# Kernel optimization log

Hardware: AMD Instinct MI355X
Metric: run time of the kernel (lower is better)

The kernel has to match this reference:

```python
import jax, jax.numpy as jnp
import numpy as np

N_NODES = 100000


def gcn_conv(x, W, b, src, dst, n_nodes):
    """PyG GCNConv: add self-loops, symmetric deg^-1/2 normalization,
    linear transform then gather->scale->scatter-add, plus bias."""
    h = x @ W  # [N, out] - transform first (small GEMM), propagate after
    loop = jnp.arange(n_nodes, dtype=src.dtype)
    s = jnp.concatenate([src, loop])  # sources incl. self-loops
    d = jnp.concatenate([dst, loop])  # targets incl. self-loops
    deg = jax.ops.segment_sum(jnp.ones_like(d, dtype=h.dtype), d,
                              num_segments=n_nodes)  # in-degree on augmented graph
    dinv = jnp.where(deg > 0, jax.lax.rsqrt(deg), 0.0)
    norm = dinv[s] * dinv[d]  # [E+N]
    msg = h[s] * norm[:, None]  # gather + per-edge scale
    out = jax.ops.segment_sum(msg, d, num_segments=n_nodes)  # scatter-add
    return out + b


def setup_inputs() -> dict:
    key = jax.random.key(0)
    ks = jax.random.split(key, 8)
    in_dim, hid = 128, 128
    n_edges = 1600000
    x = jax.random.normal(ks[0], (N_NODES, in_dim), dtype=jnp.float32)
    edge_index = jax.random.randint(ks[1], (2, n_edges), 0, N_NODES, dtype=jnp.int64)
    s1 = 1.0 / np.sqrt(in_dim)
    s2 = 1.0 / np.sqrt(hid)
    W1 = jax.random.uniform(ks[2], (in_dim, hid), jnp.float32, -s1, s1)
    b1 = jnp.zeros((hid,), jnp.float32)
    W2 = jax.random.uniform(ks[3], (hid, 2), jnp.float32, -s2, s2)
    b2 = jnp.zeros((2,), jnp.float32)
    W_skip = jax.random.uniform(ks[4], (in_dim, 2), jnp.float32, -s1, s1)
    b_skip = jnp.zeros((2,), jnp.float32)
    return {"x": x, "edge_index": edge_index, "W1": W1, "b1": b1,
            "W2": W2, "b2": b2, "W_skip": W_skip, "b_skip": b_skip}


def reference(x, edge_index, W1, b1, W2, b2, W_skip, b_skip):
    src, dst = edge_index[0], edge_index[1]
    h = gcn_conv(x, W1, b1, src, dst, N_NODES)
    h = jax.nn.relu(h)
    # dropout is identity in eval mode (training=False)
    out = gcn_conv(h, W2, b2, src, dst, N_NODES)
    out = out + x @ W_skip + b_skip
    return out
```

## Files before the change

kernel.cpp:

```cpp
#include <hip/hip_runtime.h>

#define NN 100000
#define NB 196
#define BSHIFT 9
#define BMASK 511

typedef __attribute__((ext_vector_type(8))) short short8;
typedef __attribute__((ext_vector_type(4))) float f32x4;
typedef __attribute__((ext_vector_type(2))) float f32x2;

__device__ __forceinline__ unsigned short f2bf(float f) {
  union { float f; unsigned int u; } v;
  v.f = f;
  unsigned int r = (v.u + 0x7fffu + ((v.u >> 16) & 1u)) >> 16;
  return (unsigned short)r;
}
__device__ __forceinline__ float bf_lo(unsigned int u) {
  union { unsigned int u; float f; } v;
  v.u = u << 16;
  return v.f;
}
__device__ __forceinline__ float bf_hi(unsigned int u) {
  union { unsigned int u; float f; } v;
  v.u = u & 0xffff0000u;
  return v.f;
}
__device__ __forceinline__ f32x2 bfpair(unsigned int u) {
  union { unsigned int u; float f; } lo, hi;
  lo.u = u << 16;
  hi.u = u & 0xffff0000u;
  f32x2 r;
  r.x = lo.f;
  r.y = hi.f;
  return r;
}

union SMem {
  struct {
    int cnt_l[NB];
    int start_l[NB];
    int gbase[NB];
    int wsum2[8];
    unsigned int stage[4096];
    int addr[4096];
  } b;
  struct {
    unsigned short Bs[16384];
    float Ws[256];
  } g;
};

__global__ __launch_bounds__(512) void k_phase1(const int* __restrict__ src,
                                                const int* __restrict__ dst, int E,
                                                int cap, int* __restrict__ bcur,
                                                unsigned int* __restrict__ bkt,
                                                const float* __restrict__ x,
                                                const float* __restrict__ W1,
                                                const float* __restrict__ W_skip,
                                                unsigned short* __restrict__ hA16,
                                                float* __restrict__ skipout, int N,
                                                int nbatch) {
  __shared__ __align__(16) SMem sm;
  const int t = threadIdx.x;
  const int lane = t & 63, wid = t >> 6;

  if ((int)blockIdx.x < nbatch) {
    for (int i = t; i < NB; i += 512) sm.b.cnt_l[i] = 0;
    __syncthreads();
    const int bi = blockIdx.x;
    const int e0 = bi << 12;
    unsigned int ent[8];
    int bb[8], pp[8];
#pragma unroll
    for (int j = 0; j < 8; ++j) {
      int e = e0 + j * 512 + t;
      if (e < E) {
        int d = dst[e], s = src[e];
        bb[j] = d >> BSHIFT;
        ent[j] = ((unsigned int)s << BSHIFT) | (unsigned int)(d & BMASK);
        pp[j] = atomicAdd(&sm.b.cnt_l[bb[j]], 1);
      } else {
        bb[j] = -1;
      }
    }
    __syncthreads();
    int v = (t < NB) ? sm.b.cnt_l[t] : 0;
    if (t < NB) sm.b.gbase[t] = atomicAdd(&bcur[t], v);
    int incl = v;
#pragma unroll
    for (int off = 1; off < 64; off <<= 1) {
      int u = __shfl_up(incl, off);
      if (lane >= off) incl += u;
    }
    if (lane == 63) sm.b.wsum2[wid] = incl;
    __syncthreads();
    int wpre = 0;
#pragma unroll
    for (int j = 0; j < 8; ++j) wpre += (j < wid) ? sm.b.wsum2[j] : 0;
    int tot = sm.b.wsum2[0] + sm.b.wsum2[1] + sm.b.wsum2[2] + sm.b.wsum2[3] +
              sm.b.wsum2[4] + sm.b.wsum2[5] + sm.b.wsum2[6] + sm.b.wsum2[7];
    if (t < NB) sm.b.start_l[t] = wpre + incl - v;
    __syncthreads();
#pragma unroll
    for (int j = 0; j < 8; ++j) {
      if (bb[j] >= 0) {
        int slot = sm.b.start_l[bb[j]] + pp[j];
        sm.b.stage[slot] = ent[j];
        sm.b.addr[slot] = bb[j] * cap + sm.b.gbase[bb[j]] + pp[j];
      }
    }
    __syncthreads();
    for (int s2 = t; s2 < tot; s2 += 512) bkt[sm.b.addr[s2]] = sm.b.stage[s2];
    return;
  }

  const int rb = blockIdx.x - nbatch;
#pragma unroll
  for (int it = 0; it < 4; ++it) {
    int idx = t + it * 512;
    int l2 = idx & 63, f = idx >> 6;
    int nt = f >> 2, ks = f & 3;
    int nn = nt * 16 + (l2 & 15);
    int k0 = ks * 32 + (l2 >> 4) * 8;
    unsigned short tmp[8];
#pragma unroll
    for (int j = 0; j < 8; ++j) tmp[j] = f2bf(W1[(k0 + j) * 128 + nn]);
    *(uint4*)&sm.g.Bs[idx * 8] = *(uint4*)tmp;
  }
  if (t < 256) sm.g.Ws[t] = W_skip[t];
  __syncthreads();

  const int m = lane & 15, q = lane >> 4;
  const int grow = rb * 128 + wid * 16 + m;
  const bool valid = grow < N;
  const float* xp = &x[(size_t)(valid ? grow : 0) * 128];

  f32x4 acc[8];
#pragma unroll
  for (int nt = 0; nt < 8; ++nt) acc[nt] = (f32x4){0.f, 0.f, 0.f, 0.f};
  float sk0 = 0.f, sk1 = 0.f;

#pragma unroll
  for (int ks = 0; ks < 4; ++ks) {
    short8 a;
    const int kb = ks * 32 + q * 8;
    if (valid) {
      const float* p = xp + kb;
      float4 f0 = *(const float4*)p;
      float4 f1 = *(const float4*)(p + 4);
      a[0] = (short)f2bf(f0.x); a[1] = (short)f2bf(f0.y);
      a[2] = (short)f2bf(f0.z); a[3] = (short)f2bf(f0.w);
      a[4] = (short)f2bf(f1.x); a[5] = (short)f2bf(f1.y);
      a[6] = (short)f2bf(f1.z); a[7] = (short)f2bf(f1.w);
      sk0 += f0.x * sm.g.Ws[(kb + 0) * 2] + f0.y * sm.g.Ws[(kb + 1) * 2] +
             f0.z * sm.g.Ws[(kb + 2) * 2] + f0.w * sm.g.Ws[(kb + 3) * 2] +
             f1.x * sm.g.Ws[(kb + 4) * 2] + f1.y * sm.g.Ws[(kb + 5) * 2] +
             f1.z * sm.g.Ws[(kb + 6) * 2] + f1.w * sm.g.Ws[(kb + 7) * 2];
      sk1 += f0.x * sm.g.Ws[(kb + 0) * 2 + 1] + f0.y * sm.g.Ws[(kb + 1) * 2 + 1] +
             f0.z * sm.g.Ws[(kb + 2) * 2 + 1] + f0.w * sm.g.Ws[(kb + 3) * 2 + 1] +
             f1.x * sm.g.Ws[(kb + 4) * 2 + 1] + f1.y * sm.g.Ws[(kb + 5) * 2 + 1] +
             f1.z * sm.g.Ws[(kb + 6) * 2 + 1] + f1.w * sm.g.Ws[(kb + 7) * 2 + 1];
    } else {
      a = (short8)0;
    }
#pragma unroll
    for (int nt = 0; nt < 8; ++nt) {
      short8 bfr = *(const short8*)&sm.g.Bs[((nt * 4 + ks) * 64 + lane) * 8];
      acc[nt] = __builtin_amdgcn_mfma_f32_16x16x32_bf16(a, bfr, acc[nt], 0, 0, 0);
    }
  }

  sk0 += __shfl_xor(sk0, 16); sk0 += __shfl_xor(sk0, 32);
  sk1 += __shfl_xor(sk1, 16); sk1 += __shfl_xor(sk1, 32);
  if (valid && q == 0) *(float2*)&skipout[grow * 2] = make_float2(sk0, sk1);

  const int orow = rb * 128 + wid * 16 + q * 4;
#pragma unroll
  for (int nt = 0; nt < 8; ++nt) {
    int col = nt * 16 + m;
#pragma unroll
    for (int rg = 0; rg < 4; ++rg) {
      int rr = orow + rg;
      if (rr < N) hA16[(size_t)rr * 128 + col] = f2bf(acc[nt][rg]);
    }
  }
}

__global__ __launch_bounds__(512) void k_scatter(const int* __restrict__ bcur,
                                                 const unsigned int* __restrict__ bkt,
                                                 int cap, int* __restrict__ total,
                                                 int* __restrict__ ofs,
                                                 int* __restrict__ cnt,
                                                 float* __restrict__ dinv,
                                                 int* __restrict__ bin, int n) {
  __shared__ int hist[256];
  __shared__ int sofs[256];
  __shared__ int wsum[8];
  __shared__ int base;
  const int b = blockIdx.x >> 1;
  const int sub = blockIdx.x & 1;
  const int t = threadIdx.x;
  const int lane = t & 63, wid = t >> 6;
  if (t < 256) hist[t] = 0;
  __syncthreads();
  const int m = bcur[b];
  const unsigned int* p = &bkt[(size_t)b * cap];
  for (int i = t; i < m; i += 512) {
    unsigned int u = p[i];
    int dl = u & BMASK;
    if ((dl >> 8) == sub) atomicAdd(&hist[dl & 255], 1);
  }
  __syncthreads();
  int c = (t < 256) ? hist[t] : 0;
  int cp = (c + 7) & ~7;
  int incl = cp;
#pragma unroll
  for (int off = 1; off < 64; off <<= 1) {
    int u = __shfl_up(incl, off);
    if (lane >= off) incl += u;
  }
  if (lane == 63) wsum[wid] = incl;
  __syncthreads();
  if (t == 0) {
    int run = 0;
#pragma unroll
    for (int j = 0; j < 8; ++j) { int s = wsum[j]; wsum[j] = run; run += s; }
    base = atomicAdd(total, run);
  }
  __syncthreads();
  int exc = base + wsum[wid] + incl - cp;
  if (t < 256) {
    sofs[t] = exc;
    int node = (b << BSHIFT) + (sub << 8) + t;
    if (node < n) {
      ofs[node] = exc;
      cnt[node] = c;
      dinv[node] = rsqrtf((float)c + 1.0f);
    }
    hist[t] = 0;
  }
  if (blockIdx.x == 0 && t == 300) dinv[n] = 0.f;
  __syncthreads();
  for (int p2 = c; p2 < cp; ++p2) bin[exc + p2] = n;
  for (int i = t; i < m; i += 512) {
    unsigned int u = p[i];
    int dl = u & BMASK;
    if ((dl >> 8) == sub) {
      int pos = atomicAdd(&hist[dl & 255], 1);
      bin[sofs[dl & 255] + pos] = (int)(u >> BSHIFT);
    }
  }
}

__global__ __launch_bounds__(256) void k_gather1(const int* __restrict__ ofs,
                                                 const int* __restrict__ cnt,
                                                 const int* __restrict__ bin,
                                                 const float* __restrict__ dinv,
                                                 const uint4* __restrict__ hp,
                                                 const float* __restrict__ b1,
                                                 const float* __restrict__ W2,
                                                 float* __restrict__ t2s, int N) {
  int d = blockIdx.x * 4 + (threadIdx.x >> 6);
  if (d >= N) return;
  const int lane = threadIdx.x & 63;
  const int rg = lane >> 4;
  const int fl = lane & 15;
  const int beg = ofs[d];
  const int np = (cnt[d] + 7) & ~7;

  const float dd = dinv[d];
  uint4 vs = hp[(size_t)d * 16 + fl];
  float4 b1a = *(const float4*)&b1[fl * 8];
  float4 b1b = *(const float4*)&b1[fl * 8 + 4];
  float4 wa = *(const float4*)&W2[fl * 16];
  float4 wb = *(const float4*)&W2[fl * 16 + 4];
  float4 wc = *(const float4*)&W2[fl * 16 + 8];
  float4 wd = *(const float4*)&W2[fl * 16 + 12];

  f32x2 acc2[4] = {{0.f, 0.f}, {0.f, 0.f}, {0.f, 0.f}, {0.f, 0.f}};
  for (int e0 = 0; e0 < np; e0 += 8) {
    int s0 = bin[beg + e0 + rg];
    int s1 = bin[beg + e0 + 4 + rg];
    float w0 = dinv[s0];
    float w1 = dinv[s1];
    uint4 v0 = hp[(size_t)s0 * 16 + fl];
    uint4 v1 = hp[(size_t)s1 * 16 + fl];
    acc2[0] += bfpair(v0.x) * w0;
    acc2[1] += bfpair(v0.y) * w0;
    acc2[2] += bfpair(v0.z) * w0;
    acc2[3] += bfpair(v0.w) * w0;
    acc2[0] += bfpair(v1.x) * w1;
    acc2[1] += bfpair(v1.y) * w1;
    acc2[2] += bfpair(v1.z) * w1;
    acc2[3] += bfpair(v1.w) * w1;
  }
  float acc[8];
  acc[0] = acc2[0].x; acc[1] = acc2[0].y;
  acc[2] = acc2[1].x; acc[3] = acc2[1].y;
  acc[4] = acc2[2].x; acc[5] = acc2[2].y;
  acc[6] = acc2[3].x; acc[7] = acc2[3].y;
#pragma unroll
  for (int j = 0; j < 8; ++j) {
    acc[j] += __shfl_xor(acc[j], 16);
    acc[j] += __shfl_xor(acc[j], 32);
  }
  acc[0] = fmaf(dd, bf_lo(vs.x), acc[0]); acc[1] = fmaf(dd, bf_hi(vs.x), acc[1]);
  acc[2] = fmaf(dd, bf_lo(vs.y), acc[2]); acc[3] = fmaf(dd, bf_hi(vs.y), acc[3]);
  acc[4] = fmaf(dd, bf_lo(vs.z), acc[4]); acc[5] = fmaf(dd, bf_hi(vs.z), acc[5]);
  acc[6] = fmaf(dd, bf_lo(vs.w), acc[6]); acc[7] = fmaf(dd, bf_hi(vs.w), acc[7]);

  float vj[8];
  vj[0] = fmaxf(acc[0] * dd + b1a.x, 0.f);
  vj[1] = fmaxf(acc[1] * dd + b1a.y, 0.f);
  vj[2] = fmaxf(acc[2] * dd + b1a.z, 0.f);
  vj[3] = fmaxf(acc[3] * dd + b1a.w, 0.f);
  vj[4] = fmaxf(acc[4] * dd + b1b.x, 0.f);
  vj[5] = fmaxf(acc[5] * dd + b1b.y, 0.f);
  vj[6] = fmaxf(acc[6] * dd + b1b.z, 0.f);
  vj[7] = fmaxf(acc[7] * dd + b1b.w, 0.f);
  float p0 = vj[0] * wa.x + vj[1] * wa.z + vj[2] * wb.x + vj[3] * wb.z +
             vj[4] * wc.x + vj[5] * wc.z + vj[6] * wd.x + vj[7] * wd.z;
  float p1 = vj[0] * wa.y + vj[1] * wa.w + vj[2] * wb.y + vj[3] * wb.w +
             vj[4] * wc.y + vj[5] * wc.w + vj[6] * wd.y + vj[7] * wd.w;
#pragma unroll
  for (int off = 1; off < 16; off <<= 1) {
    p0 += __shfl_xor(p0, off);
    p1 += __shfl_xor(p1, off);
  }
  if (lane == 0) *(float2*)&t2s[d * 2] = make_float2(p0 * dd, p1 * dd);
}

__global__ __launch_bounds__(256) void k_final(const float* __restrict__ b_skip,
                                               const float* __restrict__ b2,
                                               const float* __restrict__ t2s,
                                               const float* __restrict__ skipout,
                                               const float* __restrict__ dinv,
                                               const int* __restrict__ ofs,
                                               const int* __restrict__ cnt,
                                               const int* __restrict__ bin,
                                               float* __restrict__ out, int N) {
  int i = blockIdx.x * 4 + (threadIdx.x >> 6);
  if (i >= N) return;
  const int lane = threadIdx.x & 63;
  const int beg = ofs[i], end = beg + cnt[i];
  float g0 = 0.f, g1 = 0.f;
  for (int e = beg + lane; e < end; e += 64) {
    int s = bin[e];
    float2 t = *(const float2*)&t2s[s * 2];
    g0 += t.x; g1 += t.y;
  }
#pragma unroll
  for (int off = 32; off > 0; off >>= 1) {
    g0 += __shfl_down(g0, off);
    g1 += __shfl_down(g1, off);
  }
  if (lane == 0) {
    float di = dinv[i];
    float2 ts = *(const float2*)&t2s[i * 2];
    float2 sk = *(const float2*)&skipout[i * 2];
    float o0 = di * (g0 + ts.x) + b2[0] + sk.x + b_skip[0];
    float o1 = di * (g1 + ts.y) + b2[1] + sk.y + b_skip[1];
    *(float2*)&out[i * 2] = make_float2(o0, o1);
  }
}

extern "C" void kernel_launch(void* const* d_in, const int* in_sizes, int n_in,
                              void* d_out, int out_size, void* d_ws, size_t ws_size,
                              hipStream_t stream) {
  const float* x      = (const float*)d_in[0];
  const int*   edges  = (const int*)d_in[1];
  const float* W1     = (const float*)d_in[2];
  const float* b1     = (const float*)d_in[3];
  const float* W2     = (const float*)d_in[4];
  const float* b2     = (const float*)d_in[5];
  const float* W_skip = (const float*)d_in[6];
  const float* b_skip = (const float*)d_in[7];
  float* out = (float*)d_out;

  const int N = NN;
  const int E = in_sizes[1] / 2;
  const int* src = edges;
  const int* dst = edges + E;
  const size_t BINCAP = (size_t)E + 8 * (size_t)N;
  const int CAP = ((E / NB) + 896 + 255) & ~255;

  unsigned short* hA16 = (unsigned short*)d_ws;
  int*   bcur    = (int*)(hA16 + (size_t)(NN + 1) * 128);
  int*   total   = bcur + NB;
  int*   ofs     = total + 4;
  float* dinv    = (float*)(ofs + N + 4);
  int*   cnt     = (int*)(dinv + N + 8);
  unsigned int* bkt = (unsigned int*)(cnt + N);
  int*   bin     = (int*)(bkt + (size_t)NB * CAP);
  float* t2s     = (float*)(bin + BINCAP);
  float* skipout = t2s + 2 * (size_t)N;

  hipMemsetAsync(hA16 + (size_t)N * 128, 0, 256 + (NB + 4) * sizeof(int), stream);

  const int nbatch = (E + 4095) / 4096;
  const int gemmb = (N + 127) / 128;
  k_phase1<<<nbatch + gemmb, 512, 0, stream>>>(src, dst, E, CAP, bcur, bkt, x, W1,
                                               W_skip, hA16, skipout, N, nbatch);
  k_scatter<<<2 * NB, 512, 0, stream>>>(bcur, bkt, CAP, total, ofs, cnt, dinv, bin, N);
  k_gather1<<<(N + 3) / 4, 256, 0, stream>>>(ofs, cnt, bin, dinv, (const uint4*)hA16,
                                             b1, W2, t2s, N);
  k_final<<<(N + 3) / 4, 256, 0, stream>>>(b_skip, b2, t2s, skipout, dinv, ofs, cnt,
                                           bin, out, N);
}
```

Baseline: 243.3 us.

## Slice hidden features by column groups for cache-friendly layer-1 gather

Stores the bf16 hidden matrix as 8 column slices of 16 features each, and splits the layer-1 gather into per-slice blocks. Each slice is about 3.2 MB, so random neighbour reads can stay in L2/LLC instead of touching the full 25 MB matrix. The gather writes an fp32 intermediate, and a new post kernel applies bias, ReLU and the W2 projection. This adds a 51 MB write/read of that intermediate and one extra launch, and it is enabled only when the workspace is large enough.

```diff
diff --git a/kernel.cpp b/kernel.cpp
--- a/kernel.cpp
+++ b/kernel.cpp
@@ -59,7 +59,7 @@
                                                 const float* __restrict__ W_skip,
                                                 unsigned short* __restrict__ hA16,
                                                 float* __restrict__ skipout, int N,
-                                                int nbatch) {
+                                                int nbatch, int sliced) {
   __shared__ __align__(16) SMem sm;
   const int t = threadIdx.x;
   const int lane = t & 63, wid = t >> 6;
@@ -177,11 +177,16 @@
   const int orow = rb * 128 + wid * 16 + q * 4;
 #pragma unroll
   for (int nt = 0; nt < 8; ++nt) {
-    int col = nt * 16 + m;
 #pragma unroll
     for (int rg = 0; rg < 4; ++rg) {
       int rr = orow + rg;
-      if (rr < N) hA16[(size_t)rr * 128 + col] = f2bf(acc[nt][rg]);
+      if (rr < N) {
+        unsigned short hv = f2bf(acc[nt][rg]);
+        if (sliced)
+          hA16[(size_t)nt * (NN + 1) * 16 + (size_t)rr * 16 + m] = hv;
+        else
+          hA16[(size_t)rr * 128 + nt * 16 + m] = hv;
+      }
     }
   }
 }
@@ -192,7 +197,9 @@
                                                  int* __restrict__ ofs,
                                                  int* __restrict__ cnt,
                                                  float* __restrict__ dinv,
-                                                 int* __restrict__ bin, int n) {
+                                                 int* __restrict__ bin, int n,
+                                                 unsigned short* __restrict__ hS,
+                                                 int sliced) {
   __shared__ int hist[256];
   __shared__ int sofs[256];
   __shared__ int wsum[8];
@@ -239,7 +246,15 @@
     }
     hist[t] = 0;
   }
-  if (blockIdx.x == 0 && t == 300) dinv[n] = 0.f;
+  if (blockIdx.x == 0) {
+    if (t == 300) dinv[n] = 0.f;
+    if (t < 128) {
+      if (sliced)
+        hS[(size_t)(t >> 4) * (NN + 1) * 16 + (size_t)NN * 16 + (t & 15)] = 0;
+      else
+        hS[(size_t)NN * 128 + t] = 0;
+    }
+  }
   __syncthreads();
   for (int p2 = c; p2 < cp; ++p2) bin[exc + p2] = n;
   for (int i = t; i < m; i += 512) {
@@ -250,6 +265,96 @@
       bin[sofs[dl & 255] + pos] = (int)(u >> BSHIFT);
     }
   }
+}
+
+__global__ __launch_bounds__(256) void k_gather1s(const int* __restrict__ ofs,
+                                                  const int* __restrict__ cnt,
+                                                  const int* __restrict__ bin,
+                                                  const float* __restrict__ dinv,
+                                                  const unsigned short* __restrict__ hS,
+                                                  float* __restrict__ t1, int N) {
+  const int t = threadIdx.x;
+  const int slice = blockIdx.x & 7;
+  const int dbase = (blockIdx.x >> 3) * 16;
+  const int wid = t >> 6, lane = t & 63;
+  const int dq = lane >> 4;
+  const int e = (lane >> 1) & 7;
+  const int c = lane & 1;
+  const int d = dbase + wid * 4 + dq;
+  const bool ok = d < N;
+
+  const int beg = ok ? ofs[d] : 0;
+  const int np = ok ? ((cnt[d] + 7) & ~7) : 0;
+  const float dd = ok ? dinv[d] : 0.f;
+  const uint4* hp = (const uint4*)(hS + (size_t)slice * (NN + 1) * 16);
+
+  f32x2 a0 = {0.f, 0.f}, a1 = {0.f, 0.f}, a2 = {0.f, 0.f}, a3 = {0.f, 0.f};
+  for (int e0 = 0; e0 < np; e0 += 8) {
+    int sidx = bin[beg + e0 + e];
+    float w = dinv[sidx];
+    uint4 v = hp[(size_t)sidx * 2 + c];
+    a0 += bfpair(v.x) * w;
+    a1 += bfpair(v.y) * w;
+    a2 += bfpair(v.z) * w;
+    a3 += bfpair(v.w) * w;
+  }
+  float acc[8];
+  acc[0] = a0.x; acc[1] = a0.y; acc[2] = a1.x; acc[3] = a1.y;
+  acc[4] = a2.x; acc[5] = a2.y; acc[6] = a3.x; acc[7] = a3.y;
+#pragma unroll
+  for (int j = 0; j < 8; ++j) {
+    acc[j] += __shfl_xor(acc[j], 2);
+    acc[j] += __shfl_xor(acc[j], 4);
+    acc[j] += __shfl_xor(acc[j], 8);
+  }
+  if (ok && e == 0) {
+    uint4 vs = hp[(size_t)d * 2 + c];
+    acc[0] = fmaf(dd, bf_lo(vs.x), acc[0]); acc[1] = fmaf(dd, bf_hi(vs.x), acc[1]);
+    acc[2] = fmaf(dd, bf_lo(vs.y), acc[2]); acc[3] = fmaf(dd, bf_hi(vs.y), acc[3]);
+    acc[4] = fmaf(dd, bf_lo(vs.z), acc[4]); acc[5] = fmaf(dd, bf_hi(vs.z), acc[5]);
+    acc[6] = fmaf(dd, bf_lo(vs.w), acc[6]); acc[7] = fmaf(dd, bf_hi(vs.w), acc[7]);
+    float* o = &t1[(size_t)d * 128 + slice * 16 + c * 8];
+    *(float4*)o = make_float4(acc[0], acc[1], acc[2], acc[3]);
+    *(float4*)(o + 4) = make_float4(acc[4], acc[5], acc[6], acc[7]);
+  }
+}
+
+__global__ __launch_bounds__(256) void k_post(const float* __restrict__ t1,
+                                              const float* __restrict__ dinv,
+                                              const float* __restrict__ b1,
+                                              const float* __restrict__ W2,
+                                              float* __restrict__ t2s, int N) {
+  int d = blockIdx.x * 16 + (threadIdx.x >> 4);
+  if (d >= N) return;
+  const int fl = threadIdx.x & 15;
+  const float dd = dinv[d];
+  float4 va = *(const float4*)&t1[(size_t)d * 128 + fl * 8];
+  float4 vb = *(const float4*)&t1[(size_t)d * 128 + fl * 8 + 4];
+  float4 b1a = *(const float4*)&b1[fl * 8];
+  float4 b1b = *(const float4*)&b1[fl * 8 + 4];
+  float4 wa = *(const float4*)&W2[fl * 16];
+  float4 wb = *(const float4*)&W2[fl * 16 + 4];
+  float4 wc = *(const float4*)&W2[fl * 16 + 8];
+  float4 wd = *(const float4*)&W2[fl * 16 + 12];
+  float vj[8];
+  vj[0] = fmaxf(va.x * dd + b1a.x, 0.f);
+  vj[1] = fmaxf(va.y * dd + b1a.y, 0.f);
+  vj[2] = fmaxf(va.z * dd + b1a.z, 0.f);
+  vj[3] = fmaxf(va.w * dd + b1a.w, 0.f);
+  vj[4] = fmaxf(vb.x * dd + b1b.x, 0.f);
+  vj[5] = fmaxf(vb.y * dd + b1b.y, 0.f);
+  vj[6] = fmaxf(vb.z * dd + b1b.z, 0.f);
+  vj[7] = fmaxf(vb.w * dd + b1b.w, 0.f);
+  float p0 = vj[0] * wa.x + vj[1] * wa.z + vj[2] * wb.x + vj[3] * wb.z +
+             vj[4] * wc.x + vj[5] * wc.z + vj[6] * wd.x + vj[7] * wd.z;
+  float p1 = vj[0] * wa.y + vj[1] * wa.w + vj[2] * wb.y + vj[3] * wb.w +
+             vj[4] * wc.y + vj[5] * wc.w + vj[6] * wd.y + vj[7] * wd.w;
+#pragma unroll
+  for (int off = 1; off < 16; off <<= 1) {
+    p0 += __shfl_xor(p0, off);
+    p1 += __shfl_xor(p1, off);
+  }
+  if (fl == 0) *(float2*)&t2s[d * 2] = make_float2(p0 * dd, p1 * dd);
 }
 
 __global__ __launch_bounds__(256) void k_gather1(const int* __restrict__ ofs,
@@ -394,16 +499,28 @@
   int*   bin     = (int*)(bkt + (size_t)NB * CAP);
   float* t2s     = (float*)(bin + BINCAP);
   float* skipout = t2s + 2 * (size_t)N;
+  float* t1      = skipout + 2 * (size_t)N;
+
+  const size_t need = (size_t)((char*)(t1 + (size_t)N * 128) - (char*)d_ws);
+  const int sliced = (ws_size >= need) ? 1 : 0;
 
   hipMemsetAsync(hA16 + (size_t)N * 128, 0, 256 + (NB + 4) * sizeof(int), stream);
 
   const int nbatch = (E + 4095) / 4096;
   const int gemmb = (N + 127) / 128;
   k_phase1<<<nbatch + gemmb, 512, 0, stream>>>(src, dst, E, CAP, bcur, bkt, x, W1,
-                                               W_skip, hA16, skipout, N, nbatch);
-  k_scatter<<<2 * NB, 512, 0, stream>>>(bcur, bkt, CAP, total, ofs, cnt, dinv, bin, N);
-  k_gather1<<<(N + 3) / 4, 256, 0, stream>>>(ofs, cnt, bin, dinv, (const uint4*)hA16,
-                                             b1, W2, t2s, N);
+                                               W_skip, hA16, skipout, N, nbatch,
+                                               sliced);
+  k_scatter<<<2 * NB, 512, 0, stream>>>(bcur, bkt, CAP, total, ofs, cnt, dinv, bin,
+                                        N, hA16, sliced);
+  if (sliced) {
+    const int dblocks = (N + 15) / 16;
+    k_gather1s<<<dblocks * 8, 256, 0, stream>>>(ofs, cnt, bin, dinv, hA16, t1, N);
+    k_post<<<dblocks, 256, 0, stream>>>(t1, dinv, b1, W2, t2s, N);
+  } else {
+    k_gather1<<<(N + 3) / 4, 256, 0, stream>>>(ofs, cnt, bin, dinv,
+                                               (const uint4*)hA16, b1, W2, t2s, N);
+  }
   k_final<<<(N + 3) / 4, 256, 0, stream>>>(b_skip, b2, t2s, skipout, dinv, ofs, cnt,
                                            bin, out, N);
 }
```

Measured after the change: 339.5 us. 39.5% more time.

## Pre-scale GEMM output rows by source dinv to drop per-edge gather of dinv

Applied to the files above, without the earlier changes.

Adds a separate atomic in-degree kernel so the first-layer GEMM epilogue can multiply each row of h by deg^-1/2 before storing it as bf16. The first gather kernel then sums pre-scaled rows without loading dinv[src] per edge, removing one dependent random load and multiply per edge. The cost is an extra memset, an extra kernel launch with 1.6M global atomics, and reuse of the cnt buffer, which k_scatter presumably overwrites later.

```diff
diff --git a/kernel.cpp b/kernel.cpp
--- a/kernel.cpp
+++ b/kernel.cpp
@@ -50,6 +50,13 @@
   } g;
 };
 
+__global__ __launch_bounds__(256) void k_deg(const int* __restrict__ dst, int E,
+                                             int* __restrict__ deg) {
+  int i = blockIdx.x * 256 + threadIdx.x;
+  const int stride = gridDim.x * 256;
+  for (; i < E; i += stride) atomicAdd(&deg[dst[i]], 1);
+}
+
 __global__ __launch_bounds__(512) void k_phase1(const int* __restrict__ src,
                                                 const int* __restrict__ dst, int E,
                                                 int cap, int* __restrict__ bcur,
@@ -59,7 +66,8 @@
                                                 const float* __restrict__ W_skip,
                                                 unsigned short* __restrict__ hA16,
                                                 float* __restrict__ skipout, int N,
-                                                int nbatch) {
+                                                int nbatch,
+                                                const int* __restrict__ deg) {
   __shared__ __align__(16) SMem sm;
   const int t = threadIdx.x;
   const int lane = t & 63, wid = t >> 6;
@@ -175,13 +183,19 @@
   if (valid && q == 0) *(float2*)&skipout[grow * 2] = make_float2(sk0, sk1);
 
   const int orow = rb * 128 + wid * 16 + q * 4;
+  float dr[4];
+#pragma unroll
+  for (int rg = 0; rg < 4; ++rg) {
+    int rr = orow + rg;
+    dr[rg] = (rr < N) ? rsqrtf((float)deg[rr] + 1.0f) : 0.f;
+  }
 #pragma unroll
   for (int nt = 0; nt < 8; ++nt) {
     int col = nt * 16 + m;
 #pragma unroll
     for (int rg = 0; rg < 4; ++rg) {
       int rr = orow + rg;
-      if (rr < N) hA16[(size_t)rr * 128 + col] = f2bf(acc[nt][rg]);
+      if (rr < N) hA16[(size_t)rr * 128 + col] = f2bf(acc[nt][rg] * dr[rg]);
     }
   }
 }
@@ -281,18 +295,16 @@
   for (int e0 = 0; e0 < np; e0 += 8) {
     int s0 = bin[beg + e0 + rg];
     int s1 = bin[beg + e0 + 4 + rg];
-    float w0 = dinv[s0];
-    float w1 = dinv[s1];
     uint4 v0 = hp[(size_t)s0 * 16 + fl];
     uint4 v1 = hp[(size_t)s1 * 16 + fl];
-    acc2[0] += bfpair(v0.x) * w0;
-    acc2[1] += bfpair(v0.y) * w0;
-    acc2[2] += bfpair(v0.z) * w0;
-    acc2[3] += bfpair(v0.w) * w0;
-    acc2[0] += bfpair(v1.x) * w1;
-    acc2[1] += bfpair(v1.y) * w1;
-    acc2[2] += bfpair(v1.z) * w1;
-    acc2[3] += bfpair(v1.w) * w1;
+    acc2[0] += bfpair(v0.x);
+    acc2[1] += bfpair(v0.y);
+    acc2[2] += bfpair(v0.z);
+    acc2[3] += bfpair(v0.w);
+    acc2[0] += bfpair(v1.x);
+    acc2[1] += bfpair(v1.y);
+    acc2[2] += bfpair(v1.z);
+    acc2[3] += bfpair(v1.w);
   }
   float acc[8];
   acc[0] = acc2[0].x; acc[1] = acc2[0].y;
@@ -304,10 +316,10 @@
     acc[j] += __shfl_xor(acc[j], 16);
     acc[j] += __shfl_xor(acc[j], 32);
   }
-  acc[0] = fmaf(dd, bf_lo(vs.x), acc[0]); acc[1] = fmaf(dd, bf_hi(vs.x), acc[1]);
-  acc[2] = fmaf(dd, bf_lo(vs.y), acc[2]); acc[3] = fmaf(dd, bf_hi(vs.y), acc[3]);
-  acc[4] = fmaf(dd, bf_lo(vs.z), acc[4]); acc[5] = fmaf(dd, bf_hi(vs.z), acc[5]);
-  acc[6] = fmaf(dd, bf_lo(vs.w), acc[6]); acc[7] = fmaf(dd, bf_hi(vs.w), acc[7]);
+  acc[0] += bf_lo(vs.x); acc[1] += bf_hi(vs.x);
+  acc[2] += bf_lo(vs.y); acc[3] += bf_hi(vs.y);
+  acc[4] += bf_lo(vs.z); acc[5] += bf_hi(vs.z);
+  acc[6] += bf_lo(vs.w); acc[7] += bf_hi(vs.w);
 
   float vj[8];
   vj[0] = fmaxf(acc[0] * dd + b1a.x, 0.f);
@@ -396,11 +408,14 @@
   float* skipout = t2s + 2 * (size_t)N;
 
   hipMemsetAsync(hA16 + (size_t)N * 128, 0, 256 + (NB + 4) * sizeof(int), stream);
+  hipMemsetAsync(cnt, 0, (size_t)N * sizeof(int), stream);
 
   const int nbatch = (E + 4095) / 4096;
   const int gemmb = (N + 127) / 128;
+  k_deg<<<2048, 256, 0, stream>>>(dst, E, cnt);
   k_phase1<<<nbatch + gemmb, 512, 0, stream>>>(src, dst, E, CAP, bcur, bkt, x, W1,
-                                               W_skip, hA16, skipout, N, nbatch);
+                                               W_skip, hA16, skipout, N, nbatch,
+                                               cnt);
   k_scatter<<<2 * NB, 512, 0, stream>>>(bcur, bkt, CAP, total, ofs, cnt, dinv, bin, N);
   k_gather1<<<(N + 3) / 4, 256, 0, stream>>>(ofs, cnt, bin, dinv, (const uint4*)hA16,
                                              b1, W2, t2s, N);
```

New measurement: 308.1 us. 26.6% more time.
